# Performance work log

Hardware: AMD Instinct MI355X
Metric: run time of the kernel (lower is better)

## Reference

```python
import jax, jax.numpy as jnp
import numpy as np

B, S, D = 32, 64, 16
OUT_F = 8
IN_DIM = S * D                      # 1024
N_QUAD = (IN_DIM + IN_DIM ** 2) // 2  # 524800 upper-triangular (incl. diag) entries
OUT_DIM = OUT_F * S                 # 512

# Static upper-triangular indices (row-major, includes diagonal) — same order as
# torch.triu_indices(in_dim, in_dim).
_TRIU_R, _TRIU_C = np.triu_indices(IN_DIM)


def setup_inputs() -> dict:
    key = jax.random.key(0)
    k1, k2, k3 = jax.random.split(key, 3)
    input_ = jax.random.normal(k1, (B, S, D), dtype=jnp.float32)
    in_total = IN_DIM + N_QUAD
    bound = 1.0 / np.sqrt(in_total)
    W = jax.random.uniform(k2, (OUT_DIM, in_total), dtype=jnp.float32, minval=-bound, maxval=bound)
    b = jax.random.uniform(k3, (OUT_DIM,), dtype=jnp.float32, minval=-bound, maxval=bound)
    return {"input_": input_, "W": W, "b": b}


def reference(input_, W, b):
    Bsz = input_.shape[0]
    x_flat = input_.reshape(Bsz, IN_DIM)                     # [B, in_dim]
    r = jnp.asarray(_TRIU_R)
    c = jnp.asarray(_TRIU_C)
    # Quadratic features: upper-triangular entries of outer(x, x) without
    # materializing the full [B, in_dim, in_dim] outer product.
    x_squared = x_flat[:, r] * x_flat[:, c]                  # [B, N_QUAD]
    x = jnp.concatenate([x_flat, x_squared], axis=-1)        # [B, in_dim + N_QUAD]
    out = x @ W.T + b                                        # [B, out_f * S]
    return out.reshape(Bsz, S, OUT_F)
```

## Files before the change

kernel.cpp:

```cpp
#include <hip/hip_runtime.h>
#include <hip/hip_bf16.h>

#define B_SZ     32
#define IN_DIM   1024
#define K_TOTAL  525824
#define OUT_DIM  512
#define NCH      4108
#define KGN      128
#define F_BYTES  ((size_t)NCH * 8192)
#define P_ELEMS  ((size_t)KGN * B_SZ * OUT_DIM)
#define NEED_WS  (F_BYTES + P_ELEMS * 4)

typedef __attribute__((ext_vector_type(8))) short bfrag;
typedef __attribute__((ext_vector_type(4))) float f32x4;

#define GLD16(g, l) __builtin_amdgcn_global_load_lds(                      \
    (const __attribute__((address_space(1))) void*)(g),                    \
    (__attribute__((address_space(3))) void*)(l), 16, 0, 0)

__device__ inline unsigned bf16r(float f)
{
    unsigned u = __builtin_bit_cast(unsigned, f);
    return (u + 0x7FFFu + ((u >> 16) & 1u)) >> 16;
}
__device__ inline unsigned pk2(float a, float b)
{
    return bf16r(a) | (bf16r(b) << 16);
}

__global__ void bias_init_kernel(const float* __restrict__ bias, float* __restrict__ out)
{
    int i = blockIdx.x * 256 + threadIdx.x;
    out[i] = bias[i & (OUT_DIM - 1)];
}

__global__ __launch_bounds__(256)
void feat_pack_kernel(const float* __restrict__ x, int4* __restrict__ fp)
{
    const int chunk = blockIdx.x;
    const int tid   = threadIdx.x;

    #pragma unroll
    for (int i = 0; i < 2; ++i) {
        const int unit = tid + i * 256;
        const int kb   = unit >> 5;
        const int b    = unit & 31;
        const int k0   = chunk * 128 + kb * 8;
        const float* xb = x + b * IN_DIM;

        float v[8];
        if (chunk < 8) {
            #pragma unroll
            for (int e = 0; e < 8; ++e) v[e] = xb[k0 + e];
        } else {
            int t = k0 - IN_DIM;
            float disc = 4198401.0f - 8.0f * (float)t;
            int r = (int)((2049.0f - sqrtf(disc)) * 0.5f);
            int off = r * IN_DIM - ((r * (r - 1)) >> 1);
            if (t < off) { --r; off = r * IN_DIM - ((r * (r - 1)) >> 1); }
            else if (t >= off + (IN_DIM - r)) { off += IN_DIM - r; ++r; }
            int c_ = r + (t - off);
            #pragma unroll
            for (int e = 0; e < 8; ++e) {
                v[e] = xb[r] * xb[c_];
                if (c_ == IN_DIM - 1) { ++r; c_ = r; } else { ++c_; }
            }
        }
        int4 pk;
        pk.x = (int)pk2(v[0], v[1]);
        pk.y = (int)pk2(v[2], v[3]);
        pk.z = (int)pk2(v[4], v[5]);
        pk.w = (int)pk2(v[6], v[7]);
        fp[(size_t)chunk * 512 + unit] = pk;
    }
}

__global__ __launch_bounds__(256, 2)
void qgemm_mfma_kernel(const int4* __restrict__ fp,
                       const float* __restrict__ W,
                       float* __restrict__ partial)
{
    __shared__ int4 wlds[2][64][32];
    __shared__ int4 fbuf[2][512];

    const int tid  = threadIdx.x;
    const int lane = tid & 63;
    const int wv_  = tid >> 6;
    const int lrow = lane & 15;
    const int lkb  = lane >> 4;

    const int og = blockIdx.x >> 7;
    const int kg = blockIdx.x & (KGN - 1);

    const int o_blk  = og * 64;
    const int o_base = o_blk + wv_ * 16;

    f32x4 acc0 = {0.f, 0.f, 0.f, 0.f};
    f32x4 acc1 = {0.f, 0.f, 0.f, 0.f};

    #define WSTAGE(s, cc)                                                       \
    do {                                                                        \
        _Pragma("unroll")                                                       \
        for (int j_ = 0; j_ < 8; ++j_) {                                        \
            const int rl_ = 2 * j_ + (lane >> 5);                               \
            const char* src_ = (const char*)(W                                  \
                + (size_t)(o_blk + wv_ * 16 + rl_) * K_TOTAL                    \
                + (size_t)(cc) * 128)                                           \
                + (((lane & 31) << 4) ^ ((rl_ & 7) << 4));                      \
            GLD16(src_, (char*)&wlds[s][wv_ * 16 + 2 * j_][0]);                 \
        }                                                                       \
    } while (0)

    #define FSTAGE(s, cc)                                                       \
    do {                                                                        \
        const char* gp_ = (const char*)fp + (size_t)(cc) * 8192                 \
                        + wv_ * 2048 + (size_t)(lane << 4);                     \
        GLD16(gp_,        (char*)&fbuf[s][0] + wv_ * 2048);                     \
        GLD16(gp_ + 1024, (char*)&fbuf[s][0] + wv_ * 2048 + 1024);              \
    } while (0)

    #define COMPUTE(s)                                                          \
    do {                                                                        \
        const int r_  = wv_ * 16 + lrow;                                        \
        const int s7_ = lrow & 7;                                               \
        _Pragma("unroll")                                                       \
        for (int q_ = 0; q_ < 4; ++q_) {                                        \
            const int sl_ = lkb * 2 + q_ * 8;                                   \
            const float4 f0_ = __builtin_bit_cast(float4, wlds[s][r_][sl_ ^ s7_]);       \
            const float4 f1_ = __builtin_bit_cast(float4, wlds[s][r_][(sl_ + 1) ^ s7_]); \
            int4 tw_;                                                           \
            tw_.x = (int)pk2(f0_.x, f0_.y);                                     \
            tw_.y = (int)pk2(f0_.z, f0_.w);                                     \
            tw_.z = (int)pk2(f1_.x, f1_.y);                                     \
            tw_.w = (int)pk2(f1_.z, f1_.w);                                     \
            const bfrag bw_ = __builtin_bit_cast(bfrag, tw_);                   \
            const int ub_ = (q_ * 4 + lkb) * 32 + lrow;                         \
            const bfrag a0_ = __builtin_bit_cast(bfrag, fbuf[s][ub_]);          \
            const bfrag a1_ = __builtin_bit_cast(bfrag, fbuf[s][ub_ + 16]);     \
            acc0 = __builtin_amdgcn_mfma_f32_16x16x32_bf16(a0_, bw_, acc0, 0, 0, 0); \
            acc1 = __builtin_amdgcn_mfma_f32_16x16x32_bf16(a1_, bw_, acc1, 0, 0, 0); \
        }                                                                       \
    } while (0)

    const int n = (kg < 12) ? 33 : 32;
    int c = kg;

    WSTAGE(0, c);       FSTAGE(0, c);
    WSTAGE(1, c + KGN); FSTAGE(1, c + KGN);

    for (int t = 0; t < n; ++t) {
        if (t < n - 1)
            asm volatile("s_waitcnt vmcnt(10)" ::: "memory");
        else
            asm volatile("s_waitcnt vmcnt(0)" ::: "memory");
        __builtin_amdgcn_s_barrier();
        COMPUTE(t & 1);
        __builtin_amdgcn_s_barrier();
        if (t + 2 < n) {
            WSTAGE(t & 1, c + 2 * KGN);
            FSTAGE(t & 1, c + 2 * KGN);
        }
        c += KGN;
    }

    #undef COMPUTE
    #undef FSTAGE
    #undef WSTAGE

    float* pb = partial + (size_t)kg * (B_SZ * OUT_DIM) + o_base + lrow;
    const int r0 = lkb * 4;
    #pragma unroll
    for (int r = 0; r < 4; ++r) {
        pb[(size_t)(r0 + r) * OUT_DIM]      = acc0[r];
        pb[(size_t)(16 + r0 + r) * OUT_DIM] = acc1[r];
    }
}

__global__ __launch_bounds__(256)
void reduce_kernel(const float* __restrict__ partial,
                   const float* __restrict__ bias,
                   float* __restrict__ out)
{
    const int idx = blockIdx.x * 256 + threadIdx.x;
    float s = bias[idx & (OUT_DIM - 1)];
    const float* p = partial + idx;
    #pragma unroll 8
    for (int kg = 0; kg < KGN; ++kg)
        s += p[(size_t)kg * (B_SZ * OUT_DIM)];
    out[idx] = s;
}

__global__ __launch_bounds__(512, 2)
void qgemm_fallback_kernel(const float* __restrict__ x,
                           const float* __restrict__ W,
                           float* __restrict__ out)
{
    __shared__ float xt[B_SZ][512];

    const int tid  = threadIdx.x;
    const int lane = tid & 63;
    const int wave = tid >> 6;
    const int bgrp = wave & 3;
    const int ogrp = wave >> 2;

    const int og  = blockIdx.x & 31;
    const int kgf = blockIdx.x >> 5;

    const int o_base = og * 16 + ogrp * 8;
    const int b_base = bgrp * 8;

    float acc[8][8];
    #pragma unroll
    for (int i = 0; i < 8; ++i)
        #pragma unroll
        for (int o = 0; o < 8; ++o) acc[i][o] = 0.f;

    const int nch = (K_TOTAL + 511) / 512;
    for (int chunk = kgf; chunk < nch; chunk += 16) {
        const int k = chunk * 512 + tid;
        __syncthreads();
        if (k < IN_DIM) {
            #pragma unroll
            for (int b = 0; b < B_SZ; ++b)
                xt[b][tid] = x[b * IN_DIM + k];
        } else {
            const int t = k - IN_DIM;
            double disc = 4198401.0 - 8.0 * (double)t;
            int r = (int)((2049.0 - sqrt(disc)) * 0.5);
            int off = r * IN_DIM - ((r * (r - 1)) >> 1);
            if (t < off) { --r; off = r * IN_DIM - ((r * (r - 1)) >> 1); }
            else if (t >= off + (IN_DIM - r)) { off += IN_DIM - r; ++r; }
            const int ccol = r + (t - off);
            #pragma unroll
            for (int b = 0; b < B_SZ; ++b)
                xt[b][tid] = x[b * IN_DIM + r] * x[b * IN_DIM + ccol];
        }
        __syncthreads();

        const float* wrow = W + (size_t)o_base * K_TOTAL + (size_t)chunk * 512;
        #pragma unroll
        for (int pass = 0; pass < 2; ++pass) {
            const int kk = pass * 256 + lane * 4;
            float4 wv[8];
            #pragma unroll
            for (int o = 0; o < 8; ++o)
                wv[o] = *(const float4*)(wrow + (size_t)o * K_TOTAL + kk);
            float4 xv[8];
            #pragma unroll
            for (int i = 0; i < 8; ++i)
                xv[i] = *(const float4*)&xt[b_base + i][kk];
            #pragma unroll
            for (int o = 0; o < 8; ++o)
                #pragma unroll
                for (int i = 0; i < 8; ++i)
                    acc[i][o] += xv[i].x * wv[o].x + xv[i].y * wv[o].y
                               + xv[i].z * wv[o].z + xv[i].w * wv[o].w;
        }
    }

    #pragma unroll
    for (int i = 0; i < 8; ++i)
        #pragma unroll
        for (int o = 0; o < 8; ++o) {
            float v = acc[i][o];
            #pragma unroll
            for (int m = 1; m < 64; m <<= 1)
                v += __shfl_xor(v, m);
            acc[i][o] = v;
        }

    if (lane == 0) {
        #pragma unroll
        for (int i = 0; i < 8; ++i)
            #pragma unroll
            for (int o = 0; o < 8; ++o)
                atomicAdd(&out[(b_base + i) * OUT_DIM + o_base + o], acc[i][o]);
    }
}

extern "C" void kernel_launch(void* const* d_in, const int* in_sizes, int n_in,
                              void* d_out, int out_size, void* d_ws, size_t ws_size,
                              hipStream_t stream)
{
    const float* x    = (const float*)d_in[0];
    const float* W    = (const float*)d_in[1];
    const float* bias = (const float*)d_in[2];
    float* out = (float*)d_out;

    if (ws_size >= NEED_WS) {
        int4*  fpk  = (int4*)d_ws;
        float* part = (float*)((char*)d_ws + F_BYTES);
        hipLaunchKernelGGL(feat_pack_kernel, dim3(NCH), dim3(256), 0, stream, x, fpk);
        hipLaunchKernelGGL(qgemm_mfma_kernel, dim3(8 * KGN), dim3(256), 0, stream,
                           fpk, W, part);
        hipLaunchKernelGGL(reduce_kernel, dim3(64), dim3(256), 0, stream,
                           part, bias, out);
    } else {
        hipLaunchKernelGGL(bias_init_kernel, dim3(64), dim3(256), 0, stream, bias, out);
        hipLaunchKernelGGL(qgemm_fallback_kernel, dim3(512), dim3(512), 0, stream,
                           x, W, out);
    }
}
```

Baseline: 280.5 us.

## Fuse quadratic feature generation into GEMM mainloop instead of prepacked buffer

Drops the separate feature-pack kernel that wrote a bf16 buffer of about 33 MB. Each GEMM block now computes its quadratic features on the fly from a small transposed copy of x and writes them straight into LDS. This removes the global write and re-read of the feature matrix, but since 8 output-group blocks share each k-chunk, the features are recomputed 8 times and the mainloop gains index math and scattered loads. The wait counts are adjusted so the mainloop now waits only for the W loads plus the LDS writes.

```diff
diff --git a/kernel.cpp b/kernel.cpp
--- a/kernel.cpp
+++ b/kernel.cpp
@@ -7,9 +7,9 @@
 #define OUT_DIM  512
 #define NCH      4108
 #define KGN      128
-#define F_BYTES  ((size_t)NCH * 8192)
-#define P_ELEMS  ((size_t)KGN * B_SZ * OUT_DIM)
-#define NEED_WS  (F_BYTES + P_ELEMS * 4)
+#define P_BYTES  ((size_t)KGN * B_SZ * OUT_DIM * 4)
+#define XT_BYTES ((size_t)IN_DIM * B_SZ * 4)
+#define NEED_WS  (P_BYTES + XT_BYTES)
 
 typedef __attribute__((ext_vector_type(8))) short bfrag;
 typedef __attribute__((ext_vector_type(4))) float f32x4;
@@ -35,48 +35,15 @@
 }
 
 __global__ __launch_bounds__(256)
-void feat_pack_kernel(const float* __restrict__ x, int4* __restrict__ fp)
-{
-    const int chunk = blockIdx.x;
-    const int tid   = threadIdx.x;
-
-    #pragma unroll
-    for (int i = 0; i < 2; ++i) {
-        const int unit = tid + i * 256;
-        const int kb   = unit >> 5;
-        const int b    = unit & 31;
-        const int k0   = chunk * 128 + kb * 8;
-        const float* xb = x + b * IN_DIM;
-
-        float v[8];
-        if (chunk < 8) {
-            #pragma unroll
-            for (int e = 0; e < 8; ++e) v[e] = xb[k0 + e];
-        } else {
-            int t = k0 - IN_DIM;
-            float disc = 4198401.0f - 8.0f * (float)t;
-            int r = (int)((2049.0f - sqrtf(disc)) * 0.5f);
-            int off = r * IN_DIM - ((r * (r - 1)) >> 1);
-            if (t < off) { --r; off = r * IN_DIM - ((r * (r - 1)) >> 1); }
-            else if (t >= off + (IN_DIM - r)) { off += IN_DIM - r; ++r; }
-            int c_ = r + (t - off);
-            #pragma unroll
-            for (int e = 0; e < 8; ++e) {
-                v[e] = xb[r] * xb[c_];
-                if (c_ == IN_DIM - 1) { ++r; c_ = r; } else { ++c_; }
-            }
-        }
-        int4 pk;
-        pk.x = (int)pk2(v[0], v[1]);
-        pk.y = (int)pk2(v[2], v[3]);
-        pk.z = (int)pk2(v[4], v[5]);
-        pk.w = (int)pk2(v[6], v[7]);
-        fp[(size_t)chunk * 512 + unit] = pk;
-    }
+void xpose_kernel(const float* __restrict__ x, float* __restrict__ xT)
+{
+    const int idx = blockIdx.x * 256 + threadIdx.x;
+    const int k = idx >> 5, b = idx & 31;
+    xT[idx] = x[b * IN_DIM + k];
 }
 
 __global__ __launch_bounds__(256, 2)
-void qgemm_mfma_kernel(const int4* __restrict__ fp,
+void qgemm_mfma_kernel(const float* __restrict__ xT,
                        const float* __restrict__ W,
                        float* __restrict__ partial)
 {
@@ -111,12 +78,40 @@
         }                                                                       \
     } while (0)
 
-    #define FSTAGE(s, cc)                                                       \
+    #define FCOMP(s, cc)                                                        \
     do {                                                                        \
-        const char* gp_ = (const char*)fp + (size_t)(cc) * 8192                 \
-                        + wv_ * 2048 + (size_t)(lane << 4);                     \
-        GLD16(gp_,        (char*)&fbuf[s][0] + wv_ * 2048);                     \
-        GLD16(gp_ + 1024, (char*)&fbuf[s][0] + wv_ * 2048 + 1024);              \
+        _Pragma("unroll")                                                       \
+        for (int i_ = 0; i_ < 2; ++i_) {                                        \
+            const int u_  = tid + i_ * 256;           \
+            const int kb_ = u_ >> 5;                                            \
+            const int b_  = u_ & 31;                                            \
+            const int k0_ = (cc) * 128 + kb_ * 8;                               \
+            float v_[8];                                                        \
+            if (k0_ < IN_DIM) {                                                 \
+                _Pragma("unroll")                                               \
+                for (int e_ = 0; e_ < 8; ++e_)                                  \
+                    v_[e_] = xT[(k0_ + e_) * B_SZ + b_];                        \
+            } else {                                                            \
+                int t_ = k0_ - IN_DIM;                                          \
+                float disc_ = 4198401.0f - 8.0f * (float)t_;                    \
+                int r_ = (int)((2049.0f - sqrtf(disc_)) * 0.5f);                \
+                int off_ = r_ * IN_DIM - ((r_ * (r_ - 1)) >> 1);                \
+                if (t_ < off_) { --r_; off_ = r_ * IN_DIM - ((r_ * (r_ - 1)) >> 1); } \
+                else if (t_ >= off_ + (IN_DIM - r_)) { off_ += IN_DIM - r_; ++r_; }   \
+                int c2_ = r_ + (t_ - off_);                                     \
+                _Pragma("unroll")                                               \
+                for (int e_ = 0; e_ < 8; ++e_) {                                \
+                    v_[e_] = xT[r_ * B_SZ + b_] * xT[c2_ * B_SZ + b_];          \
+                    if (c2_ == IN_DIM - 1) { ++r_; c2_ = r_; } else { ++c2_; }  \
+                }                                                               \
+            }                                                                   \
+            int4 pk_;                                                           \
+            pk_.x = (int)pk2(v_[0], v_[1]);                                     \
+            pk_.y = (int)pk2(v_[2], v_[3]);                                     \
+            pk_.z = (int)pk2(v_[4], v_[5]);                                     \
+            pk_.w = (int)pk2(v_[6], v_[7]);                                     \
+            fbuf[s][u_] = pk_;                                                  \
+        }                                                                       \
     } while (0)
 
     #define COMPUTE(s)                                                          \
@@ -145,26 +140,28 @@
     const int n = (kg < 12) ? 33 : 32;
     int c = kg;
 
-    WSTAGE(0, c);       FSTAGE(0, c);
-    WSTAGE(1, c + KGN); FSTAGE(1, c + KGN);
+    WSTAGE(0, c);
+    WSTAGE(1, c + KGN);
+    FCOMP(0, c);
+    FCOMP(1, c + KGN);
 
     for (int t = 0; t < n; ++t) {
         if (t < n - 1)
-            asm volatile("s_waitcnt vmcnt(10)" ::: "memory");
+            asm volatile("s_waitcnt vmcnt(8) lgkmcnt(0)" ::: "memory");
         else
-            asm volatile("s_waitcnt vmcnt(0)" ::: "memory");
+            asm volatile("s_waitcnt vmcnt(0) lgkmcnt(0)" ::: "memory");
         __builtin_amdgcn_s_barrier();
         COMPUTE(t & 1);
         __builtin_amdgcn_s_barrier();
         if (t + 2 < n) {
             WSTAGE(t & 1, c + 2 * KGN);
-            FSTAGE(t & 1, c + 2 * KGN);
+            FCOMP(t & 1, c + 2 * KGN);
         }
         c += KGN;
     }
 
     #undef COMPUTE
-    #undef FSTAGE
+    #undef FCOMP
     #undef WSTAGE
 
     float* pb = partial + (size_t)kg * (B_SZ * OUT_DIM) + o_base + lrow;
@@ -288,11 +285,11 @@
     float* out = (float*)d_out;
 
     if (ws_size >= NEED_WS) {
-        int4*  fpk  = (int4*)d_ws;
-        float* part = (float*)((char*)d_ws + F_BYTES);
-        hipLaunchKernelGGL(feat_pack_kernel, dim3(NCH), dim3(256), 0, stream, x, fpk);
+        float* part = (float*)d_ws;
+        float* xT   = (float*)((char*)d_ws + P_BYTES);
+        hipLaunchKernelGGL(xpose_kernel, dim3(128), dim3(256), 0, stream, x, xT);
         hipLaunchKernelGGL(qgemm_mfma_kernel, dim3(8 * KGN), dim3(256), 0, stream,
-                           fpk, W, part);
+                           xT, W, part);
         hipLaunchKernelGGL(reduce_kernel, dim3(64), dim3(256), 0, stream,
                            part, bias, out);
     } else {
```

After: 256.8 us, median of 2. 8.5% less time.

## Give each wave private LDS buffers and drop barriers; cut split-K to 32 segments

Applied to the files above, without the earlier changes.

Each wave now owns its own W and feature LDS staging buffers and loads all 8 feature vectors itself, so the two block-wide barriers per iteration are removed. Synchronisation relies only on per-wave vmcnt waits. The split-K factor drops from 128 to 32, so the grid shrinks to 256 blocks with 128 iterations each and the reduce kernel sums fewer partials. In exchange the feature data is loaded four times per block, LDS use grows, and with only 256 blocks of one occupancy slot the GPU may be underfilled, which could hurt memory-latency hiding.

```diff
diff --git a/kernel.cpp b/kernel.cpp
--- a/kernel.cpp
+++ b/kernel.cpp
@@ -6,10 +6,10 @@
 #define K_TOTAL  525824
 #define OUT_DIM  512
 #define NCH      4108
-#define KGN      128
+#define KSEG     32
 #define F_BYTES  ((size_t)NCH * 8192)
-#define P_ELEMS  ((size_t)KGN * B_SZ * OUT_DIM)
-#define NEED_WS  (F_BYTES + P_ELEMS * 4)
+#define P_BYTES  ((size_t)KSEG * B_SZ * OUT_DIM * 4)
+#define NEED_WS  (F_BYTES + P_BYTES)
 
 typedef __attribute__((ext_vector_type(8))) short bfrag;
 typedef __attribute__((ext_vector_type(4))) float f32x4;
@@ -75,13 +75,13 @@
     }
 }
 
-__global__ __launch_bounds__(256, 2)
+__global__ __launch_bounds__(256, 1)
 void qgemm_mfma_kernel(const int4* __restrict__ fp,
                        const float* __restrict__ W,
                        float* __restrict__ partial)
 {
-    __shared__ int4 wlds[2][64][32];
-    __shared__ int4 fbuf[2][512];
+    __shared__ int4 wlds[4][2][16][32];
+    __shared__ int4 flds[4][2][512];
 
     const int tid  = threadIdx.x;
     const int lane = tid & 63;
@@ -89,11 +89,9 @@
     const int lrow = lane & 15;
     const int lkb  = lane >> 4;
 
-    const int og = blockIdx.x >> 7;
-    const int kg = blockIdx.x & (KGN - 1);
-
-    const int o_blk  = og * 64;
-    const int o_base = o_blk + wv_ * 16;
+    const int kseg = blockIdx.x & 31;
+    const int opos = (blockIdx.x >> 5) * 4 + wv_;
+    const int o_base = opos * 16;
 
     f32x4 acc0 = {0.f, 0.f, 0.f, 0.f};
     f32x4 acc1 = {0.f, 0.f, 0.f, 0.f};
@@ -104,30 +102,29 @@
         for (int j_ = 0; j_ < 8; ++j_) {                                        \
             const int rl_ = 2 * j_ + (lane >> 5);                               \
             const char* src_ = (const char*)(W                                  \
-                + (size_t)(o_blk + wv_ * 16 + rl_) * K_TOTAL                    \
-                + (size_t)(cc) * 128)                                           \
+                + (size_t)(o_base + rl_) * K_TOTAL + (size_t)(cc) * 128)        \
                 + (((lane & 31) << 4) ^ ((rl_ & 7) << 4));                      \
-            GLD16(src_, (char*)&wlds[s][wv_ * 16 + 2 * j_][0]);                 \
+            GLD16(src_, (char*)&wlds[wv_][s][2 * j_][0]);                       \
         }                                                                       \
     } while (0)
 
     #define FSTAGE(s, cc)                                                       \
     do {                                                                        \
         const char* gp_ = (const char*)fp + (size_t)(cc) * 8192                 \
-                        + wv_ * 2048 + (size_t)(lane << 4);                     \
-        GLD16(gp_,        (char*)&fbuf[s][0] + wv_ * 2048);                     \
-        GLD16(gp_ + 1024, (char*)&fbuf[s][0] + wv_ * 2048 + 1024);              \
+                        + (size_t)(lane << 4);                                  \
+        _Pragma("unroll")                                                       \
+        for (int j_ = 0; j_ < 8; ++j_)                                          \
+            GLD16(gp_ + j_ * 1024, (char*)&flds[wv_][s][0] + j_ * 1024);        \
     } while (0)
 
     #define COMPUTE(s)                                                          \
     do {                                                                        \
-        const int r_  = wv_ * 16 + lrow;                                        \
         const int s7_ = lrow & 7;                                               \
         _Pragma("unroll")                                                       \
         for (int q_ = 0; q_ < 4; ++q_) {                                        \
             const int sl_ = lkb * 2 + q_ * 8;                                   \
-            const float4 f0_ = __builtin_bit_cast(float4, wlds[s][r_][sl_ ^ s7_]);       \
-            const float4 f1_ = __builtin_bit_cast(float4, wlds[s][r_][(sl_ + 1) ^ s7_]); \
+            const float4 f0_ = __builtin_bit_cast(float4, wlds[wv_][s][lrow][sl_ ^ s7_]);       \
+            const float4 f1_ = __builtin_bit_cast(float4, wlds[wv_][s][lrow][(sl_ + 1) ^ s7_]); \
             int4 tw_;                                                           \
             tw_.x = (int)pk2(f0_.x, f0_.y);                                     \
             tw_.y = (int)pk2(f0_.z, f0_.w);                                     \
@@ -135,39 +132,37 @@
             tw_.w = (int)pk2(f1_.z, f1_.w);                                     \
             const bfrag bw_ = __builtin_bit_cast(bfrag, tw_);                   \
             const int ub_ = (q_ * 4 + lkb) * 32 + lrow;                         \
-            const bfrag a0_ = __builtin_bit_cast(bfrag, fbuf[s][ub_]);          \
-            const bfrag a1_ = __builtin_bit_cast(bfrag, fbuf[s][ub_ + 16]);     \
+            const bfrag a0_ = __builtin_bit_cast(bfrag, flds[wv_][s][ub_]);     \
+            const bfrag a1_ = __builtin_bit_cast(bfrag, flds[wv_][s][ub_ + 16]);\
             acc0 = __builtin_amdgcn_mfma_f32_16x16x32_bf16(a0_, bw_, acc0, 0, 0, 0); \
             acc1 = __builtin_amdgcn_mfma_f32_16x16x32_bf16(a1_, bw_, acc1, 0, 0, 0); \
         }                                                                       \
     } while (0)
 
-    const int n = (kg < 12) ? 33 : 32;
-    int c = kg;
-
-    WSTAGE(0, c);       FSTAGE(0, c);
-    WSTAGE(1, c + KGN); FSTAGE(1, c + KGN);
+    const int n = (kseg < 12) ? 129 : 128;
+    int c = kseg;
+
+    FSTAGE(0, c);        WSTAGE(0, c);
+    FSTAGE(1, c + KSEG); WSTAGE(1, c + KSEG);
 
     for (int t = 0; t < n; ++t) {
         if (t < n - 1)
-            asm volatile("s_waitcnt vmcnt(10)" ::: "memory");
+            asm volatile("s_waitcnt vmcnt(16)" ::: "memory");
         else
             asm volatile("s_waitcnt vmcnt(0)" ::: "memory");
-        __builtin_amdgcn_s_barrier();
         COMPUTE(t & 1);
-        __builtin_amdgcn_s_barrier();
         if (t + 2 < n) {
-            WSTAGE(t & 1, c + 2 * KGN);
-            FSTAGE(t & 1, c + 2 * KGN);
-        }
-        c += KGN;
+            FSTAGE(t & 1, c + 2 * KSEG);
+            WSTAGE(t & 1, c + 2 * KSEG);
+        }
+        c += KSEG;
     }
 
     #undef COMPUTE
     #undef FSTAGE
     #undef WSTAGE
 
-    float* pb = partial + (size_t)kg * (B_SZ * OUT_DIM) + o_base + lrow;
+    float* pb = partial + (size_t)kseg * (B_SZ * OUT_DIM) + o_base + lrow;
     const int r0 = lkb * 4;
     #pragma unroll
     for (int r = 0; r < 4; ++r) {
@@ -185,7 +180,7 @@
     float s = bias[idx & (OUT_DIM - 1)];
     const float* p = partial + idx;
     #pragma unroll 8
-    for (int kg = 0; kg < KGN; ++kg)
+    for (int kg = 0; kg < KSEG; ++kg)
         s += p[(size_t)kg * (B_SZ * OUT_DIM)];
     out[idx] = s;
 }
@@ -291,7 +286,7 @@
         int4*  fpk  = (int4*)d_ws;
         float* part = (float*)((char*)d_ws + F_BYTES);
         hipLaunchKernelGGL(feat_pack_kernel, dim3(NCH), dim3(256), 0, stream, x, fpk);
-        hipLaunchKernelGGL(qgemm_mfma_kernel, dim3(8 * KGN), dim3(256), 0, stream,
+        hipLaunchKernelGGL(qgemm_mfma_kernel, dim3(256), dim3(256), 0, stream,
                            fpk, W, part);
         hipLaunchKernelGGL(reduce_kernel, dim3(64), dim3(256), 0, stream,
                            part, bias, out);
```

Measured after the change: 285.8 us. About the same (+1.9%).
